# Kernel tuning notes

Hardware: AMD Instinct MI355X
Metric: run time of the kernel (lower is better)

The kernel has to match this reference:

```python
import jax, jax.numpy as jnp
import numpy as np

N = 100_000          # nodes
E = 3_200_000        # edges (avg degree 32)
H = 20               # hidden_channels (node feature width, = 10 one-hot + 10 mlp)
EH = 64              # edge_hidden_dim
EO = 10              # edge_output_dim
THRESHOLD = 1.0


def setup_inputs() -> dict:
    key = jax.random.key(0)
    ks = jax.random.split(key, 12)
    x = jax.random.normal(ks[0], (N, 2, H), dtype=jnp.float32)
    edge_index = jax.random.randint(ks[1], (2, E), 0, N, dtype=jnp.int32)
    # distances strictly in (0, threshold]
    edge_attr = jax.random.uniform(ks[2], (E, 1), jnp.float32, 1e-4, THRESHOLD)
    # parameters (torch.rand init as in the module)
    a = jax.random.uniform(ks[3], (1,), jnp.float32)
    b = jax.random.uniform(ks[4], (1,), jnp.float32) + 1.0
    gamma1 = jax.random.uniform(ks[5], (H, H), jnp.float32)
    gamma2 = jax.random.uniform(ks[6], (H, H), jnp.float32)
    bias = jax.random.uniform(ks[7], (H,), jnp.float32)
    # edge MLP: Linear(1, EH) -> ReLU -> Linear(EH, EO)
    W1 = jax.random.normal(ks[8], (1, EH), jnp.float32)
    b1 = jnp.zeros((EH,), jnp.float32)
    W2 = jax.random.normal(ks[9], (EH, EO), jnp.float32) / np.sqrt(EH)
    b2 = jnp.zeros((EO,), jnp.float32)
    return dict(x=x, edge_index=edge_index, edge_attr=edge_attr, a=a, b=b,
                gamma1=gamma1, gamma2=gamma2, bias=bias, W1=W1, b1=b1, W2=W2, b2=b2)


def reference(x, edge_index, edge_attr, a, b, gamma1, gamma2, bias, W1, b1, W2, b2):
    src, dst = edge_index[0], edge_index[1]
    # --- edge features ---
    h = jax.nn.relu(edge_attr @ W1 + b1)            # [E, EH]
    mlp_out = h @ W2 + b2                           # [E, EO]
    # one-hot distance bucket: 10 equal intervals over (0, threshold], idx 10 -> 9
    idx = jnp.clip((edge_attr[:, 0] * (10.0 / THRESHOLD)).astype(jnp.int32), 0, 9)
    one_hot = jax.nn.one_hot(idx, 10, dtype=x.dtype)  # [E, 10]
    eac = jnp.concatenate([one_hot, mlp_out], axis=1)  # edge_attr_combined [E, 20]
    # --- per-source-node normalization (w_tilde) ---
    sum_w = jax.ops.segment_sum(eac, src, num_segments=N)  # [N, 20]
    sw = sum_w[src]                                        # [E, 20]
    safe = jnp.where(sw != 0, sw, 1.0)
    w_tilde = jnp.where(sw != 0, eac / safe, jnp.asarray(0.01, x.dtype))
    # --- rho weighting on node features ---
    h_j = x[src, 0]                                  # [E, 20]
    h_jp = x[dst, 0]                                 # [E, 20]
    rho = jnp.abs(a * h_j - (1.0 - a) * h_jp) ** b   # [E, 20]
    # --- aggregate messages per source node ---
    sum_features = jax.ops.segment_sum(rho * w_tilde, src, num_segments=N)  # [N, 20]
    # --- node update ---
    out0 = jax.nn.sigmoid(x[:, 0] @ gamma1.T + sum_features @ gamma2.T + bias)
    return jnp.stack([out0, sum_features], axis=1)   # [N, 2, 20]
```

## Files before the change

### kernel.cpp

```cpp
#include <hip/hip_runtime.h>
#include <hip/hip_bf16.h>


#define BATCH 4096
#define BPT   16
#define BSH   7
#define CAP   4608

__device__ int block_scan_excl(int* data, int n, int* scratch) {
    const int t = threadIdx.x;
    const int lane = t & 63, w = t >> 6;
    const int base = t * 4;
    int v0 = (base + 0 < n) ? data[base + 0] : 0;
    int v1 = (base + 1 < n) ? data[base + 1] : 0;
    int v2 = (base + 2 < n) ? data[base + 2] : 0;
    int v3 = (base + 3 < n) ? data[base + 3] : 0;
    int p1 = v0 + v1, p2 = p1 + v2, p3 = p2 + v3;
    int x = p3;
    #pragma unroll
    for (int o = 1; o < 64; o <<= 1) { int y = __shfl_up(x, o); if (lane >= o) x += y; }
    if (lane == 63) scratch[w] = x;
    __syncthreads();
    int wbase = 0;
    for (int i = 0; i < w; ++i) wbase += scratch[i];
    int tb = wbase + x - p3;
    if (base + 0 < n) data[base + 0] = tb;
    if (base + 1 < n) data[base + 1] = tb + v0;
    if (base + 2 < n) data[base + 2] = tb + p1;
    if (base + 3 < n) data[base + 3] = tb + p2;
    int tot = scratch[0] + scratch[1] + scratch[2] + scratch[3];
    __syncthreads();
    return tot;
}

__launch_bounds__(256)
__global__ void k_bcount(const int* __restrict__ src, int* __restrict__ bcount,
                         const float* __restrict__ x, __hip_bfloat16* __restrict__ xa,
                         int E, int nb, int N) {
    __shared__ int lc[1024];
    const int t = threadIdx.x;
    for (int i = t; i < 1024; i += 256) lc[i] = 0;
    __syncthreads();
    const int base = blockIdx.x * BATCH;
    #pragma unroll
    for (int k = 0; k < BPT; ++k) {
        int e = base + k * 256 + t;
        if (e < E) atomicAdd(&lc[src[e] >> BSH], 1);
    }
    __syncthreads();
    for (int i = t; i < nb; i += 256) { int c = lc[i]; if (c) atomicAdd(&bcount[i], c); }
    const int stride = gridDim.x * 256;
    for (int i = blockIdx.x * 256 + t; i < N * 20; i += stride) {
        int n = i / 20, c = i - n * 20;
        xa[(n << 5) + c] = __float2bfloat16(x[n * 40 + c]);
    }
}

__global__ void k_bscan(int* __restrict__ bcount, int* __restrict__ bstart,
                        int* __restrict__ gcursor, int nb,
                        const float* __restrict__ W1, const float* __restrict__ b1,
                        const float* __restrict__ W2, const float* __restrict__ b2,
                        float* __restrict__ AB, int* __restrict__ flag,
                        int EH, int EO) {
    __shared__ int scratch[4];
    int total = block_scan_excl(bcount, nb, scratch);
    const int t = threadIdx.x;
    for (int i = t; i < nb; i += 256) { bstart[i] = bcount[i]; gcursor[i] = bcount[i]; }
    if (t == 0) bstart[nb] = total;
    if (t == 64) {
        int ok = 1;
        for (int k = 0; k < EH; ++k) if (b1[k] != 0.0f) ok = 0;
        *flag = ok;
    }
    if (t < EO) {
        float A = 0.0f;
        for (int k = 0; k < EH; ++k)
            if (W1[k] > 0.0f) A = fmaf(W1[k], W2[k * EO + t], A);
        AB[t]      = A;
        AB[EO + t] = b2[t];
    }
}

__launch_bounds__(256)
__global__ void k_bscatter(const int* __restrict__ src, const int* __restrict__ dst,
                           const float* __restrict__ ea, int* __restrict__ gcursor,
                           int2* __restrict__ tmp, int E, int nb) {
    __shared__ int  pay[BATCH];
    __shared__ unsigned char pbn[BATCH];
    __shared__ unsigned short sbid[BATCH];
    __shared__ int  lcount[1024];
    __shared__ int  lsave[1024];
    __shared__ int  scratch[4];
    const int t = threadIdx.x;
    for (int i = t; i < 1024; i += 256) lcount[i] = 0;
    __syncthreads();
    const int base = blockIdx.x * BATCH;
    int mys[BPT], myr[BPT], myw[BPT];
    #pragma unroll
    for (int k = 0; k < BPT; ++k) {
        int e = base + k * 256 + t;
        mys[k] = -1;
        if (e < E) {
            int s = src[e], d = dst[e];
            float dd = ea[e];
            int ib = (int)(dd * 10.0f);
            ib = ib < 0 ? 0 : (ib > 9 ? 9 : ib);
            int dq = (int)fmaf(dd, 2047.0f, 0.5f);
            dq = dq < 0 ? 0 : (dq > 2047 ? 2047 : dq);
            mys[k] = s;
            myr[k] = atomicAdd(&lcount[s >> BSH], 1);
            myw[k] = (d & 0x1FFFF) | (ib << 17) | (dq << 21);
        }
    }
    __syncthreads();
    for (int i = t; i < 1024; i += 256) lsave[i] = lcount[i];
    __syncthreads();
    int total = block_scan_excl(lcount, nb, scratch);
    for (int b = t; b < nb; b += 256) {
        int c = lsave[b];
        if (c > 0) lsave[b] = atomicAdd(&gcursor[b], c);
    }
    __syncthreads();
    #pragma unroll
    for (int k = 0; k < BPT; ++k) {
        if (mys[k] >= 0) {
            int b = mys[k] >> BSH;
            int pos = lcount[b] + myr[k];
            pay[pos]  = myw[k];
            pbn[pos]  = (unsigned char)(mys[k] & 127);
            sbid[pos] = (unsigned short)b;
        }
    }
    __syncthreads();
    for (int j = t; j < total; j += 256) {
        int b = sbid[j];
        tmp[lsave[b] + (j - lcount[b])] = make_int2(pay[j], (int)pbn[j]);
    }
}

template <int USE_XA>
__launch_bounds__(512, 8)
__global__ void k_nodeb(const float* __restrict__ x,
                        const __hip_bfloat16* __restrict__ xa,
                        const int* __restrict__ bstart,
                        const int2* __restrict__ tmp,
                        const float* __restrict__ a_p, const float* __restrict__ b_p,
                        const float* __restrict__ g1, const float* __restrict__ g2,
                        const float* __restrict__ bias,
                        const float* __restrict__ AB, const int* __restrict__ flag_p,
                        const float* __restrict__ W1, const float* __restrict__ b1,
                        const float* __restrict__ W2, const float* __restrict__ b2,
                        float* __restrict__ out, int N, int EH, int EO) {
    __shared__ int   buf[CAP];
    __shared__ int   hist[128];
    __shared__ int   rowstart[129];
    __shared__ int   lcur[128];
    __shared__ unsigned char perm[128];
    __shared__ __hip_bfloat16 s_x0[128 * 22];
    __shared__ float s_sf[128 * 21];
    __shared__ float s_g1[20 * 21], s_g2[20 * 21], s_b[20];

    const int t = threadIdx.x;
    const int b = blockIdx.x;
    const int node0 = b << BSH;
    const int s0 = bstart[b];
    const int m  = bstart[b + 1] - s0;

    if (t < 128) hist[t] = 0;
    for (int i = t; i < 400; i += 512) {
        int r = i / 20, cc = i - r * 20;
        s_g1[r * 21 + cc] = g1[i];
        s_g2[r * 21 + cc] = g2[i];
    }
    if (t < 20) s_b[t] = bias[t];
    for (int i = t; i < 2560; i += 512) {
        int l = i / 20, cc = i - l * 20;
        int n = node0 + l;
        s_x0[l * 22 + cc] = __float2bfloat16((n < N) ? x[n * 40 + cc] : 0.0f);
    }
    __syncthreads();

    int vw[9], vn[9];
    #pragma unroll
    for (int k = 0; k < 9; ++k) {
        int i = k * 512 + t;
        vn[k] = -1;
        if (i < m && i < CAP) {
            int2 v = tmp[s0 + i];
            vw[k] = v.x;
            vn[k] = v.y & 127;
            atomicAdd(&hist[vn[k]], 1);
        }
    }
    __syncthreads();
    if (t < 64) {
        int a = hist[2 * t], bb = hist[2 * t + 1];
        int s = a + bb;
        int xsc = s;
        #pragma unroll
        for (int o = 1; o < 64; o <<= 1) { int y = __shfl_up(xsc, o); if (t >= o) xsc += y; }
        int excl = xsc - s;
        rowstart[2 * t]     = excl;
        rowstart[2 * t + 1] = excl + a;
        lcur[2 * t]         = excl;
        lcur[2 * t + 1]     = excl + a;
        if (t == 63) rowstart[128] = xsc;
    }
    __syncthreads();
    #pragma unroll
    for (int k = 0; k < 9; ++k) {
        if (vn[k] >= 0) {
            int p = atomicAdd(&lcur[vn[k]], 1);
            if (p < CAP) buf[p] = vw[k];
        }
    }
    __syncthreads();

    if (t < 128) hist[t] = 0;
    __syncthreads();
    if (t < 128) {
        int len = rowstart[t + 1] - rowstart[t];
        int bin = 127 - (len > 127 ? 127 : len);
        atomicAdd(&hist[bin], 1);
    }
    __syncthreads();
    if (t < 64) {
        int a = hist[2 * t], bb = hist[2 * t + 1];
        int s = a + bb;
        int xsc = s;
        #pragma unroll
        for (int o = 1; o < 64; o <<= 1) { int y = __shfl_up(xsc, o); if (t >= o) xsc += y; }
        int excl = xsc - s;
        hist[2 * t]     = excl;
        hist[2 * t + 1] = excl + a;
    }
    __syncthreads();
    if (t < 128) {
        int len = rowstart[t + 1] - rowstart[t];
        int bin = 127 - (len > 127 ? 127 : len);
        int pos = atomicAdd(&hist[bin], 1);
        perm[pos] = (unsigned char)t;
    }

    const float av = a_p[0], bv = b_p[0];
    const float am1 = 1.0f - av;
    const int fl = *flag_p;
    __syncthreads();

    #pragma unroll
    for (int r = 0; r < 5; ++r) {
        int item = t + 512 * r;
        int li = perm[item / 20];
        int c = item - (item / 20) * 20;
        const bool cl10 = c < 10;
        float x0c = __bfloat162float(s_x0[li * 22 + c]);
        const float pax = av * x0c;
        int rs = rowstart[li];
        int re = rowstart[li + 1];
        float sf;
        if (fl || cl10) {
            float sA = 0.0f, sB = 0.0f, s2 = 0.0f;
            int i = rs;
            for (; i + 4 <= re; i += 4) {
                int w0 = buf[i + 0];
                int w1 = buf[i + 1];
                int w2 = buf[i + 2];
                int w3 = buf[i + 3];
                float xd0, xd1, xd2, xd3;
                if (USE_XA) {
                    xd0 = __bfloat162float(xa[((w0 & 0x1FFFF) << 5) + c]);
                    xd1 = __bfloat162float(xa[((w1 & 0x1FFFF) << 5) + c]);
                    xd2 = __bfloat162float(xa[((w2 & 0x1FFFF) << 5) + c]);
                    xd3 = __bfloat162float(xa[((w3 & 0x1FFFF) << 5) + c]);
                } else {
                    xd0 = x[(w0 & 0x1FFFF) * 40 + c];
                    xd1 = x[(w1 & 0x1FFFF) * 40 + c];
                    xd2 = x[(w2 & 0x1FFFF) * 40 + c];
                    xd3 = x[(w3 & 0x1FFFF) * 40 + c];
                }
                #define STEP(w_, xd_)                                          \
                {                                                              \
                    float tt_  = fabsf(fmaf(-am1, (xd_), pax));                \
                    float rho_ = exp2f(bv * __log2f(tt_));                     \
                    int   ib_  = ((w_) >> 17) & 0xF;                           \
                    float dqf_ = (float)(((unsigned)(w_)) >> 21);              \
                    float sel_ = cl10 ? ((ib_ == c) ? 1.0f : 0.0f) : dqf_;     \
                    sA += sel_;                                                \
                    sB = fmaf(rho_, sel_, sB);                                 \
                    s2 += rho_;                                                \
                }
                STEP(w0, xd0); STEP(w1, xd1); STEP(w2, xd2); STEP(w3, xd3);
            }
            for (; i < re; ++i) {
                int w0 = buf[i];
                float xd0 = USE_XA ? __bfloat162float(xa[((w0 & 0x1FFFF) << 5) + c])
                                   : x[(w0 & 0x1FFFF) * 40 + c];
                STEP(w0, xd0);
            }
            float sw, s1;
            if (cl10) { sw = sA; s1 = sB; }
            else {
                float Afq = AB[c - 10] * (1.0f / 2047.0f);
                float Bf  = AB[c];
                float deg = (float)(re - rs);
                sw = fmaf(Afq, sA, Bf * deg);
                s1 = fmaf(Afq, sB, Bf * s2);
            }
            sf = (sw != 0.0f) ? (s1 / sw) : (0.01f * s2);
        } else {
            float sw = 0.0f, s1 = 0.0f, s2 = 0.0f;
            for (int i = rs; i < re; ++i) {
                int w0 = buf[i];
                float xd0 = USE_XA ? __bfloat162float(xa[((w0 & 0x1FFFF) << 5) + c])
                                   : x[(w0 & 0x1FFFF) * 40 + c];
                float dd_ = (float)(((unsigned)w0) >> 21) * (1.0f / 2047.0f);
                float m_ = b2[c - 10];
                for (int k_ = 0; k_ < EH; ++k_) {
                    float h_ = fmaf(dd_, W1[k_], b1[k_]);
                    h_ = h_ > 0.0f ? h_ : 0.0f;
                    m_ = fmaf(h_, W2[k_ * EO + (c - 10)], m_);
                }
                float tt_  = fabsf(fmaf(-am1, xd0, pax));
                float rho_ = exp2f(bv * __log2f(tt_));
                sw += m_;
                s1 = fmaf(rho_, m_, s1);
                s2 += rho_;
            }
            sf = (sw != 0.0f) ? (s1 / sw) : (0.01f * s2);
        }
        s_sf[li * 21 + c] = sf;
    }
    __syncthreads();

    for (int i = t; i < 2560; i += 512) {
        int l = i / 20, cc = i - l * 20;
        int n = node0 + l;
        if (n < N) {
            float acc = s_b[cc];
            const __hip_bfloat16* xr = &s_x0[l * 22];
            const float* sr  = &s_sf[l * 21];
            const float* g1r = &s_g1[cc * 21];
            const float* g2r = &s_g2[cc * 21];
            #pragma unroll
            for (int k = 0; k < 20; ++k)
                acc = fmaf(__bfloat162float(xr[k]), g1r[k], fmaf(sr[k], g2r[k], acc));
            float o0 = 1.0f / (1.0f + __expf(-acc));
            out[n * 40 + cc]      = o0;
            out[n * 40 + 20 + cc] = sr[cc];
        }
    }
}

extern "C" void kernel_launch(void* const* d_in, const int* in_sizes, int n_in,
                              void* d_out, int out_size, void* d_ws, size_t ws_size,
                              hipStream_t stream) {
    const float* x    = (const float*)d_in[0];
    const int*   ei   = (const int*)  d_in[1];
    const float* ea   = (const float*)d_in[2];
    const float* a_p  = (const float*)d_in[3];
    const float* b_p  = (const float*)d_in[4];
    const float* g1   = (const float*)d_in[5];
    const float* g2   = (const float*)d_in[6];
    const float* bias = (const float*)d_in[7];
    const float* W1   = (const float*)d_in[8];
    const float* b1   = (const float*)d_in[9];
    const float* W2   = (const float*)d_in[10];
    const float* b2   = (const float*)d_in[11];
    float* out = (float*)d_out;

    const int E  = in_sizes[2];
    const int N  = in_sizes[0] / 40;
    const int EH = in_sizes[8];
    const int EO = in_sizes[11];
    const int* src = ei;
    const int* dst = ei + E;

    const int nb     = (N + 127) >> BSH;
    const int nbatch = (E + BATCH - 1) / BATCH;

    int* ws_i = (int*)d_ws;
    size_t o = 0;
    int* bcount  = ws_i + o; o += (size_t)nb;       o = (o + 1) & ~(size_t)1;
    int* bstart  = ws_i + o; o += (size_t)(nb + 1); o = (o + 1) & ~(size_t)1;
    int* gcursor = ws_i + o; o += (size_t)nb;       o = (o + 1) & ~(size_t)1;
    float* AB    = (float*)(ws_i + o); o += 2 * (size_t)EO;
    int* flag    = ws_i + o; o += 1;                o = (o + 1) & ~(size_t)1;
    int2* tmp    = (int2*)(ws_i + o); o += 2 * (size_t)E;
    __hip_bfloat16* xa = (__hip_bfloat16*)(ws_i + o);
    const size_t need_xa = o * 4 + (size_t)N * 32 * 2;
    const int use_xa = (ws_size >= need_xa) ? 1 : 0;

    hipMemsetAsync(bcount, 0, (size_t)nb * sizeof(int), stream);

    k_bcount  <<<nbatch, 256, 0, stream>>>(src, bcount, x, use_xa ? xa : (__hip_bfloat16*)AB,
                                           E, nb, use_xa ? N : 0);
    k_bscan   <<<1,      256, 0, stream>>>(bcount, bstart, gcursor, nb,
                                           W1, b1, W2, b2, AB, flag, EH, EO);
    k_bscatter<<<nbatch, 256, 0, stream>>>(src, dst, ea, gcursor, tmp, E, nb);
    if (use_xa) {
        k_nodeb<1><<<nb, 512, 0, stream>>>(x, xa, bstart, tmp, a_p, b_p,
                                           g1, g2, bias, AB, flag,
                                           W1, b1, W2, b2, out, N, EH, EO);
    } else {
        k_nodeb<0><<<nb, 512, 0, stream>>>(x, xa, bstart, tmp, a_p, b_p,
                                           g1, g2, bias, AB, flag,
                                           W1, b1, W2, b2, out, N, EH, EO);
    }
}
```

Baseline: 257.1 us.

## Replace global bucket count/scan with per-batch offset table gathered by node blocks

```diff
diff --git a/kernel.cpp b/kernel.cpp
--- a/kernel.cpp
+++ b/kernel.cpp
@@ -33,61 +33,42 @@
     return tot;
 }
 
+__global__ void k_init(const float* __restrict__ x, __hip_bfloat16* __restrict__ xa,
+                       int N, int do_xa,
+                       const float* __restrict__ W1, const float* __restrict__ b1,
+                       const float* __restrict__ W2, const float* __restrict__ b2,
+                       float* __restrict__ AB, int* __restrict__ flag,
+                       int EH, int EO) {
+    const int t = threadIdx.x;
+    if (blockIdx.x == 0) {
+        if (t == 64) {
+            int ok = 1;
+            for (int k = 0; k < EH; ++k) if (b1[k] != 0.0f) ok = 0;
+            *flag = ok;
+        }
+        if (t < EO) {
+            float A = 0.0f;
+            for (int k = 0; k < EH; ++k)
+                if (W1[k] > 0.0f) A = fmaf(W1[k], W2[k * EO + t], A);
+            AB[t]      = A;
+            AB[EO + t] = b2[t];
+        }
+    }
+    if (do_xa) {
+        const int stride = gridDim.x * blockDim.x;
+        for (int i = blockIdx.x * blockDim.x + t; i < N * 20; i += stride) {
+            int n = i / 20, c = i - n * 20;
+            xa[(n << 5) + c] = __float2bfloat16(x[n * 40 + c]);
+        }
+    }
+}
+
 __launch_bounds__(256)
-__global__ void k_bcount(const int* __restrict__ src, int* __restrict__ bcount,
-                         const float* __restrict__ x, __hip_bfloat16* __restrict__ xa,
-                         int E, int nb, int N) {
-    __shared__ int lc[1024];
-    const int t = threadIdx.x;
-    for (int i = t; i < 1024; i += 256) lc[i] = 0;
-    __syncthreads();
-    const int base = blockIdx.x * BATCH;
-    #pragma unroll
-    for (int k = 0; k < BPT; ++k) {
-        int e = base + k * 256 + t;
-        if (e < E) atomicAdd(&lc[src[e] >> BSH], 1);
-    }
-    __syncthreads();
-    for (int i = t; i < nb; i += 256) { int c = lc[i]; if (c) atomicAdd(&bcount[i], c); }
-    const int stride = gridDim.x * 256;
-    for (int i = blockIdx.x * 256 + t; i < N * 20; i += stride) {
-        int n = i / 20, c = i - n * 20;
-        xa[(n << 5) + c] = __float2bfloat16(x[n * 40 + c]);
-    }
-}
-
-__global__ void k_bscan(int* __restrict__ bcount, int* __restrict__ bstart,
-                        int* __restrict__ gcursor, int nb,
-                        const float* __restrict__ W1, const float* __restrict__ b1,
-                        const float* __restrict__ W2, const float* __restrict__ b2,
-                        float* __restrict__ AB, int* __restrict__ flag,
-                        int EH, int EO) {
-    __shared__ int scratch[4];
-    int total = block_scan_excl(bcount, nb, scratch);
-    const int t = threadIdx.x;
-    for (int i = t; i < nb; i += 256) { bstart[i] = bcount[i]; gcursor[i] = bcount[i]; }
-    if (t == 0) bstart[nb] = total;
-    if (t == 64) {
-        int ok = 1;
-        for (int k = 0; k < EH; ++k) if (b1[k] != 0.0f) ok = 0;
-        *flag = ok;
-    }
-    if (t < EO) {
-        float A = 0.0f;
-        for (int k = 0; k < EH; ++k)
-            if (W1[k] > 0.0f) A = fmaf(W1[k], W2[k * EO + t], A);
-        AB[t]      = A;
-        AB[EO + t] = b2[t];
-    }
-}
-
-__launch_bounds__(256)
-__global__ void k_bscatter(const int* __restrict__ src, const int* __restrict__ dst,
-                           const float* __restrict__ ea, int* __restrict__ gcursor,
-                           int2* __restrict__ tmp, int E, int nb) {
+__global__ void k_bscat(const int* __restrict__ src, const int* __restrict__ dst,
+                        const float* __restrict__ ea, int2* __restrict__ tmp,
+                        unsigned* __restrict__ table, int E, int nb) {
     __shared__ int  pay[BATCH];
     __shared__ unsigned char pbn[BATCH];
-    __shared__ unsigned short sbid[BATCH];
     __shared__ int  lcount[1024];
     __shared__ int  lsave[1024];
     __shared__ int  scratch[4];
@@ -116,41 +97,35 @@
     for (int i = t; i < 1024; i += 256) lsave[i] = lcount[i];
     __syncthreads();
     int total = block_scan_excl(lcount, nb, scratch);
-    for (int b = t; b < nb; b += 256) {
-        int c = lsave[b];
-        if (c > 0) lsave[b] = atomicAdd(&gcursor[b], c);
-    }
-    __syncthreads();
+    for (int b = t; b < nb; b += 256)
+        table[blockIdx.x * nb + b] = (unsigned)lcount[b] | ((unsigned)lsave[b] << 16);
     #pragma unroll
     for (int k = 0; k < BPT; ++k) {
         if (mys[k] >= 0) {
             int b = mys[k] >> BSH;
             int pos = lcount[b] + myr[k];
-            pay[pos]  = myw[k];
-            pbn[pos]  = (unsigned char)(mys[k] & 127);
-            sbid[pos] = (unsigned short)b;
-        }
-    }
-    __syncthreads();
-    for (int j = t; j < total; j += 256) {
-        int b = sbid[j];
-        tmp[lsave[b] + (j - lcount[b])] = make_int2(pay[j], (int)pbn[j]);
-    }
+            pay[pos] = myw[k];
+            pbn[pos] = (unsigned char)(mys[k] & 127);
+        }
+    }
+    __syncthreads();
+    for (int j = t; j < total; j += 256)
+        tmp[base + j] = make_int2(pay[j], (int)pbn[j]);
 }
 
 template <int USE_XA>
 __launch_bounds__(512, 8)
 __global__ void k_nodeb(const float* __restrict__ x,
                         const __hip_bfloat16* __restrict__ xa,
-                        const int* __restrict__ bstart,
                         const int2* __restrict__ tmp,
+                        const unsigned* __restrict__ table, int nbatch,
                         const float* __restrict__ a_p, const float* __restrict__ b_p,
                         const float* __restrict__ g1, const float* __restrict__ g2,
                         const float* __restrict__ bias,
                         const float* __restrict__ AB, const int* __restrict__ flag_p,
                         const float* __restrict__ W1, const float* __restrict__ b1,
                         const float* __restrict__ W2, const float* __restrict__ b2,
-                        float* __restrict__ out, int N, int EH, int EO) {
+                        float* __restrict__ out, int N, int nb, int EH, int EO) {
     __shared__ int   buf[CAP];
     __shared__ int   hist[128];
     __shared__ int   rowstart[129];
@@ -163,8 +138,6 @@
     const int t = threadIdx.x;
     const int b = blockIdx.x;
     const int node0 = b << BSH;
-    const int s0 = bstart[b];
-    const int m  = bstart[b + 1] - s0;
 
     if (t < 128) hist[t] = 0;
     for (int i = t; i < 400; i += 512) {
@@ -180,17 +153,13 @@
     }
     __syncthreads();
 
-    int vw[9], vn[9];
-    #pragma unroll
-    for (int k = 0; k < 9; ++k) {
-        int i = k * 512 + t;
-        vn[k] = -1;
-        if (i < m && i < CAP) {
-            int2 v = tmp[s0 + i];
-            vw[k] = v.x;
-            vn[k] = v.y & 127;
-            atomicAdd(&hist[vn[k]], 1);
-        }
+    const int* tmpi = (const int*)tmp;
+    for (int i = t; i < nbatch; i += 512) {
+        unsigned ent = table[i * nb + b];
+        int off = (int)(ent & 0xFFFFu), cnt = (int)(ent >> 16);
+        int base2 = 2 * (i * BATCH + off) + 1;
+        for (int k = 0; k < cnt; ++k)
+            atomicAdd(&hist[tmpi[base2 + 2 * k] & 127], 1);
     }
     __syncthreads();
     if (t < 64) {
@@ -207,11 +176,14 @@
         if (t == 63) rowstart[128] = xsc;
     }
     __syncthreads();
-    #pragma unroll
-    for (int k = 0; k < 9; ++k) {
-        if (vn[k] >= 0) {
-            int p = atomicAdd(&lcur[vn[k]], 1);
-            if (p < CAP) buf[p] = vw[k];
+    for (int i = t; i < nbatch; i += 512) {
+        unsigned ent = table[i * nb + b];
+        int off = (int)(ent & 0xFFFFu), cnt = (int)(ent >> 16);
+        const int2* p = tmp + i * BATCH + off;
+        for (int k = 0; k < cnt; ++k) {
+            int2 v = p[k];
+            int pp = atomicAdd(&lcur[v.y & 127], 1);
+            if (pp < CAP) buf[pp] = v.x;
         }
     }
     __syncthreads();
@@ -257,6 +229,8 @@
         const float pax = av * x0c;
         int rs = rowstart[li];
         int re = rowstart[li + 1];
+        if (re > CAP) re = CAP;
+        if (rs > re) rs = re;
         float sf;
         if (fl || cl10) {
             float sA = 0.0f, sB = 0.0f, s2 = 0.0f;
@@ -380,30 +354,25 @@
 
     int* ws_i = (int*)d_ws;
     size_t o = 0;
-    int* bcount  = ws_i + o; o += (size_t)nb;       o = (o + 1) & ~(size_t)1;
-    int* bstart  = ws_i + o; o += (size_t)(nb + 1); o = (o + 1) & ~(size_t)1;
-    int* gcursor = ws_i + o; o += (size_t)nb;       o = (o + 1) & ~(size_t)1;
-    float* AB    = (float*)(ws_i + o); o += 2 * (size_t)EO;
-    int* flag    = ws_i + o; o += 1;                o = (o + 1) & ~(size_t)1;
-    int2* tmp    = (int2*)(ws_i + o); o += 2 * (size_t)E;
+    float* AB     = (float*)(ws_i + o); o += 2 * (size_t)EO;
+    int* flag     = ws_i + o; o += 1;
+    unsigned* table = (unsigned*)(ws_i + o); o += (size_t)nbatch * nb;
+    o = (o + 1) & ~(size_t)1;
+    int2* tmp     = (int2*)(ws_i + o); o += 2 * (size_t)nbatch * BATCH;
     __hip_bfloat16* xa = (__hip_bfloat16*)(ws_i + o);
     const size_t need_xa = o * 4 + (size_t)N * 32 * 2;
     const int use_xa = (ws_size >= need_xa) ? 1 : 0;
 
-    hipMemsetAsync(bcount, 0, (size_t)nb * sizeof(int), stream);
-
-    k_bcount  <<<nbatch, 256, 0, stream>>>(src, bcount, x, use_xa ? xa : (__hip_bfloat16*)AB,
-                                           E, nb, use_xa ? N : 0);
-    k_bscan   <<<1,      256, 0, stream>>>(bcount, bstart, gcursor, nb,
-                                           W1, b1, W2, b2, AB, flag, EH, EO);
-    k_bscatter<<<nbatch, 256, 0, stream>>>(src, dst, ea, gcursor, tmp, E, nb);
+    k_init <<<256,    256, 0, stream>>>(x, xa, N, use_xa, W1, b1, W2, b2,
+                                        AB, flag, EH, EO);
+    k_bscat<<<nbatch, 256, 0, stream>>>(src, dst, ea, tmp, table, E, nb);
     if (use_xa) {
-        k_nodeb<1><<<nb, 512, 0, stream>>>(x, xa, bstart, tmp, a_p, b_p,
+        k_nodeb<1><<<nb, 512, 0, stream>>>(x, xa, tmp, table, nbatch, a_p, b_p,
                                            g1, g2, bias, AB, flag,
-                                           W1, b1, W2, b2, out, N, EH, EO);
+                                           W1, b1, W2, b2, out, N, nb, EH, EO);
     } else {
-        k_nodeb<0><<<nb, 512, 0, stream>>>(x, xa, bstart, tmp, a_p, b_p,
+        k_nodeb<0><<<nb, 512, 0, stream>>>(x, xa, tmp, table, nbatch, a_p, b_p,
                                            g1, g2, bias, AB, flag,
-                                           W1, b1, W2, b2, out, N, EH, EO);
-    }
-}
+                                           W1, b1, W2, b2, out, N, nb, EH, EO);
+    }
+}
```

Result: slower. 276.5 us (+7.6%).
